# Kernel tuning notes

Hardware: AMD Instinct MI355X
Metric: run time of the kernel (lower is better)

## Reference

```python
import math
import jax, jax.numpy as jnp
import numpy as np

T, D, H, HD, ETA, R = 4096, 1024, 8, 64, 4, 7
EPS = 1e-5


def _discounted_sum(start_state, x, discounts):
    """state[t] = state[t-1]*discounts[t] + x[t], scanned over leading axis T."""
    def step(s, xd):
        xt, dt = xd
        s = s * dt + xt
        return s, s
    _, ys = jax.lax.scan(step, start_state, (x, discounts))
    return ys  # (T, *)


def _forward(inputs, terminations, tilde_k_prev, tilde_v_prev, s_prev, tick,
             W_kqv, b_kqv, W_p, b_p, W_proj, b_proj):
    cur_seq = inputs.shape[0]
    term = terminations.astype(inputs.dtype)

    kqv = (inputs @ W_kqv + b_kqv).reshape(cur_seq, H, 5 * HD)
    keys, queries, values, beta, gammas = jnp.split(kqv, 5, axis=-1)  # each (T,H,HD)
    p = (inputs @ W_p + b_p).reshape(cur_seq, H, 3 * ETA)
    p1, p2, p3 = jnp.split(p, 3, axis=-1)  # each (T,H,ETA)

    # feature-map expansion: outer product over (eta, head_dim) -> flatten to eta*HD
    keys = jnp.einsum('chd,chn->chnd', jax.nn.relu(keys), jax.nn.relu(p1)).reshape(cur_seq, H, ETA * HD)
    queries = jnp.einsum('chd,chn->chnd', jax.nn.relu(queries), jax.nn.relu(p2)).reshape(cur_seq, H, ETA * HD)
    gammas = jnp.einsum('chd,chn->chnd', jax.nn.sigmoid(gammas), jax.nn.sigmoid(p3)).reshape(cur_seq, H, ETA * HD)
    beta = jax.nn.sigmoid(beta)  # (T,H,HD)

    ticks = tick.reshape(1, 1) + jnp.arange(1, cur_seq + 1, dtype=inputs.dtype).reshape(-1, 1)  # (T,1)->(T,R)
    omegas = jnp.linspace(-math.pi, math.pi, R).astype(inputs.dtype).reshape(1, -1)
    occil = jnp.cos(ticks * omegas)  # (T,R)

    values = values * beta
    values = values[:, None, :, :] * occil[:, :, None, None]  # (T,R,H,HD)
    keys = keys * gammas
    s = keys  # (T,H,ETA*HD)
    keys = keys[:, None, :, :] * occil[:, :, None, None]  # (T,R,H,ETA*HD)

    not_term = (1.0 - term).reshape(cur_seq, 1, 1)
    discount_gamma = (1.0 - gammas) * not_term  # (T,H,ETA*HD)
    discount_beta = (1.0 - beta) * not_term     # (T,H,HD)

    final_keys = _discounted_sum(tilde_k_prev, keys, discount_gamma[:, None])    # (T,R,H,ETA*HD)
    final_values = _discounted_sum(tilde_v_prev, values, discount_beta[:, None])  # (T,R,H,HD)
    final_s = _discounted_sum(s_prev, s, discount_gamma)                          # (T,H,ETA*HD)

    kdq = jnp.einsum('crhd,chd->crh', final_keys, queries)
    kv = jnp.einsum('crhd,crh->chd', final_values, kdq)  # sum over r
    norm = jnp.einsum('chd,chd->ch', final_s, queries)
    attn_out = kv / (2 * R * norm[..., None] + EPS)
    attn_out = attn_out.reshape(cur_seq, H * HD) @ W_proj + b_proj  # dropout p=0.0 is identity

    new_tick = tick + cur_seq
    return attn_out, final_keys[-1], final_values[-1], final_s[-1], new_tick


def setup_inputs() -> dict:
    key = jax.random.key(0)
    ks = jax.random.split(key, 5)
    return {
        'inputs': jax.random.normal(ks[0], (T, D), jnp.float32),
        'terminations': jax.random.randint(ks[1], (T,), 0, 2, jnp.int32),
        'tilde_k_prev': jnp.zeros((R, H, ETA * HD), jnp.float32),
        'tilde_v_prev': jnp.zeros((R, H, HD), jnp.float32),
        's_prev': jnp.zeros((H, ETA * HD), jnp.float32),
        'tick': jnp.ones((1,), jnp.float32),
        'W_kqv': jax.random.normal(ks[2], (D, H * HD * 5), jnp.float32) * 0.02,
        'b_kqv': jnp.zeros((H * HD * 5,), jnp.float32),
        'W_p': jax.random.normal(ks[3], (D, H * ETA * 3), jnp.float32) * 0.02,
        'b_p': jnp.zeros((H * ETA * 3,), jnp.float32),
        'W_proj': jax.random.normal(ks[4], (H * HD, D), jnp.float32) * 0.02,
        'b_proj': jnp.zeros((D,), jnp.float32),
    }


def reference(inputs, terminations, tilde_k_prev, tilde_v_prev, s_prev, tick,
              W_kqv, b_kqv, W_p, b_p, W_proj, b_proj):
    return _forward(inputs, terminations, tilde_k_prev, tilde_v_prev, s_prev, tick,
                    W_kqv, b_kqv, W_p, b_p, W_proj, b_proj)
```

## Files before the change

### kernel.cpp

```cpp
#include <hip/hip_runtime.h>
#include <hip/hip_bf16.h>
#include <math.h>

#define T_SEQ 4096
#define DIM   1024
#define NH    8
#define HDIM  64
#define ETA   4
#define NR    7
#define NKQVC 2688
#define CHUNK 16
#define NCHUNK 256

typedef __attribute__((ext_vector_type(8))) short bf16x8;
typedef __attribute__((ext_vector_type(4))) short short4v;
typedef __attribute__((ext_vector_type(4))) float f32x4;

#define KQVC_OFF    0ul
#define OCC_OFF     5505024ul
#define BTPROJ_OFF  5537792ul
#define ATTNBF_OFF  5799936ul
#define BIASC_OFF   6848512ul
#define ABF_OFF     6851328ul
#define BTCAT_OFF   8948480ul
#define YSUM_OFF    6851328ul

#define O_ATTN 0ul
#define O_FK   4194304ul
#define O_FV   4208640ul
#define O_FS   4212224ul
#define O_TICK 4214272ul

__device__ __forceinline__ float sigm(float x) { return 1.f / (1.f + __expf(-x)); }

__device__ __forceinline__ short f2bf(float f) {
  union { __hip_bfloat16 b; short s; } u;
  u.b = __float2bfloat16(f);
  return u.s;
}
__device__ __forceinline__ float bf2f(short s) {
  union { __hip_bfloat16 b; short s2; } u;
  u.s2 = s;
  return __bfloat162float(u.b);
}

__device__ __forceinline__ void gload16(const void* g, void* l) {
  __builtin_amdgcn_global_load_lds(
      (const __attribute__((address_space(1))) void*)g,
      (__attribute__((address_space(3))) void*)l, 16, 0, 0);
}

__global__ __launch_bounds__(256) void cast_f32_bf16(
    const float* __restrict__ x, short* __restrict__ y) {
  size_t i = (size_t)(blockIdx.x * 256 + threadIdx.x) * 4;
  float4 v = *(const float4*)(x + i);
  short4v o;
  o.x = f2bf(v.x); o.y = f2bf(v.y); o.z = f2bf(v.z); o.w = f2bf(v.w);
  *(short4v*)(y + i) = o;
}

__global__ __launch_bounds__(256) void transpose_cast(
    const float* __restrict__ W, short* __restrict__ Bt, int K, int N) {
  __shared__ float tile[32][33];
  int n0 = blockIdx.x * 32, k0 = blockIdx.y * 32;
  int tx = threadIdx.x, ty = threadIdx.y;
  for (int i = ty; i < 32; i += 8)
    tile[i][tx] = W[(size_t)(k0 + i) * N + n0 + tx];
  __syncthreads();
  for (int i = ty; i < 32; i += 8)
    Bt[(size_t)(n0 + i) * K + k0 + tx] = f2bf(tile[tx][i]);
}

__global__ __launch_bounds__(256) void concat_bias(
    const float* __restrict__ b_kqv, const float* __restrict__ b_p,
    float* __restrict__ bc) {
  int i = blockIdx.x * 256 + threadIdx.x;
  if (i >= NKQVC) return;
  bc[i] = (i < 2560) ? b_kqv[i] : (i < 2656 ? b_p[i - 2560] : 0.f);
}

template <int OUT_BF16>
__global__ __launch_bounds__(256) void gemm_bt_mfma(
    const short* __restrict__ A, const short* __restrict__ Bt,
    const float* __restrict__ bias, void* __restrict__ Cout,
    int M, int N, int K) {
  __shared__ __align__(16) short lds[16384];

  int nwg = gridDim.x;
  int cpx = nwg >> 3;
  int bid = blockIdx.x;
  int swz = (bid & 7) * cpx + (bid >> 3);
  int nbx = N >> 7;
  int bm0 = (swz / nbx) << 7;
  int bn0 = (swz % nbx) << 7;

  const int tid = threadIdx.x;
  const int w = tid >> 6, l = tid & 63;
  const int wm = w >> 1, wn = w & 1;
  const int fr = l & 15;
  const int fq = l >> 4;

  const int ca = w * 2;
  const short* Ag0 = A + (size_t)(bm0 + ca * 16 + (l >> 2)) * K + (l & 3) * 8;
  const short* Ag1 = Ag0 + (size_t)16 * K;
  const short* Bg0 = Bt + (size_t)(bn0 + ca * 16 + (l >> 2)) * K + (l & 3) * 8;
  const short* Bg1 = Bg0 + (size_t)16 * K;

  f32x4 acc[4][4];
#pragma unroll
  for (int mi = 0; mi < 4; ++mi)
#pragma unroll
    for (int ni = 0; ni < 4; ++ni)
#pragma unroll
      for (int r = 0; r < 4; ++r) acc[mi][ni][r] = 0.f;

  const int KT = K >> 5;
  int cur = 0;
  {
    short* la = &lds[ca * 512];
    short* lb = &lds[4096 + ca * 512];
    gload16(Ag0, la);
    gload16(Ag1, la + 512);
    gload16(Bg0, lb);
    gload16(Bg1, lb + 512);
  }
  __syncthreads();

  for (int kt = 0; kt < KT; ++kt) {
    if (kt + 1 < KT) {
      int nb = (cur ^ 1) * 8192;
      int ko = (kt + 1) * 32;
      short* la = &lds[nb + ca * 512];
      short* lb = &lds[nb + 4096 + ca * 512];
      gload16(Ag0 + ko, la);
      gload16(Ag1 + ko, la + 512);
      gload16(Bg0 + ko, lb);
      gload16(Bg1 + ko, lb + 512);
    }
    const short* ArP = &lds[cur * 8192 + (wm * 64 + fr) * 32 + fq * 8];
    const short* BrP = &lds[cur * 8192 + 4096 + (wn * 64 + fr) * 32 + fq * 8];
    bf16x8 af[4], bfv[4];
#pragma unroll
    for (int mi = 0; mi < 4; ++mi) af[mi] = *(const bf16x8*)(ArP + mi * 512);
#pragma unroll
    for (int ni = 0; ni < 4; ++ni) bfv[ni] = *(const bf16x8*)(BrP + ni * 512);
#pragma unroll
    for (int mi = 0; mi < 4; ++mi)
#pragma unroll
      for (int ni = 0; ni < 4; ++ni)
        acc[mi][ni] = __builtin_amdgcn_mfma_f32_16x16x32_bf16(
            af[mi], bfv[ni], acc[mi][ni], 0, 0, 0);
    __syncthreads();
    cur ^= 1;
  }

  if (OUT_BF16) {
#pragma unroll
    for (int ni = 0; ni < 4; ++ni) {
      int col = wn * 64 + ni * 16 + fr;
      float bz = bias[bn0 + col];
#pragma unroll
      for (int mi = 0; mi < 4; ++mi) {
        int row = wm * 64 + mi * 16 + fq * 4;
#pragma unroll
        for (int r = 0; r < 4; ++r)
          lds[(row + r) * 128 + col] = f2bf(acc[mi][ni][r] + bz);
      }
    }
    __syncthreads();
    int row = tid >> 1, half = tid & 1;
    const f32x4* src = (const f32x4*)&lds[row * 128 + half * 64];
    f32x4* dst = (f32x4*)((short*)Cout + (size_t)(bm0 + row) * N + bn0 + half * 64);
#pragma unroll
    for (int i = 0; i < 8; ++i) dst[i] = src[i];
  } else {
#pragma unroll
    for (int ni = 0; ni < 4; ++ni) {
      int col = bn0 + wn * 64 + ni * 16 + fr;
      float bz = bias[col];
#pragma unroll
      for (int mi = 0; mi < 4; ++mi) {
        int row = bm0 + wm * 64 + mi * 16 + fq * 4;
#pragma unroll
        for (int r = 0; r < 4; ++r)
          ((float*)Cout)[(size_t)(row + r) * N + col] = acc[mi][ni][r] + bz;
      }
    }
  }
}

__global__ __launch_bounds__(256) void occil_kernel(const float* __restrict__ tick,
                                                    float* __restrict__ occ) {
  int t = blockIdx.x * 256 + threadIdx.x;
  if (t >= T_SEQ) return;
  float tickt = tick[0] + (float)(t + 1);
#pragma unroll
  for (int r = 0; r < NR; ++r) {
    float om = (float)(-3.14159265358979323846 + r * (3.14159265358979323846 / 3.0));
    occ[t * 8 + r] = cosf(tickt * om);
  }
  occ[t * 8 + 7] = 0.f;
}

__global__ __launch_bounds__(128) void pass_a(
    const short* __restrict__ kqv, const float* __restrict__ occ,
    const int* __restrict__ term, float* __restrict__ ysum) {
  const int c = blockIdx.x, h = blockIdx.y;
  const int tid = threadIdx.x;
  const int w = tid >> 6, dd = tid & 63;
  const int R0 = w ? 4 : 0;
  const int RN = w ? 3 : 4;
  __shared__ float sp[CHUNK][12];
  __shared__ float socc[CHUNK][8];
  __shared__ float snt[CHUNK];
  for (int i = tid; i < CHUNK * 12; i += 128) {
    int t = i / 12, j = i - t * 12;
    sp[t][j] = bf2f(kqv[(size_t)(c * CHUNK + t) * NKQVC + 2560 + h * 12 + j]);
  }
  for (int i = tid; i < CHUNK * 8; i += 128)
    socc[i >> 3][i & 7] = occ[(size_t)c * CHUNK * 8 + i];
  for (int t = tid; t < CHUNK; t += 128)
    snt[t] = 1.f - (float)term[c * CHUNK + t];
  __syncthreads();

  float yk[4][ETA], yv[4], ys[ETA], Pg[ETA], Pb = 1.f;
#pragma unroll
  for (int rr = 0; rr < 4; ++rr) {
    yv[rr] = 0.f;
#pragma unroll
    for (int n = 0; n < ETA; ++n) yk[rr][n] = 0.f;
  }
#pragma unroll
  for (int n = 0; n < ETA; ++n) { ys[n] = 0.f; Pg[n] = 1.f; }

  size_t bcur = (size_t)(c * CHUNK) * NKQVC + h * 320 + dd;
  short ck = kqv[bcur], cv = kqv[bcur + 128], cbt = kqv[bcur + 192], cg = kqv[bcur + 256];
  for (int t = 0; t < CHUNK; ++t) {
    size_t bnx = bcur + (t < CHUNK - 1 ? NKQVC : 0);
    short nk = kqv[bnx], nv = kqv[bnx + 128], nbt = kqv[bnx + 192], ng = kqv[bnx + 256];

    float nt = snt[t];
    float rk = fmaxf(bf2f(ck), 0.f);
    float sg = sigm(bf2f(cg));
    float sb = sigm(bf2f(cbt));
    float occr[4];
#pragma unroll
    for (int rr = 0; rr < 4; ++rr) occr[rr] = socc[t][R0 + rr];
#pragma unroll
    for (int n = 0; n < ETA; ++n) {
      float rp1 = fmaxf(sp[t][n], 0.f);
      float sp3 = sigm(sp[t][8 + n]);
      float gam = sg * sp3;
      float xs  = rk * rp1 * gam;
      float dg  = (1.f - gam) * nt;
      if (w) {
        Pg[n] *= dg;
        ys[n] = fmaf(ys[n], dg, xs);
      }
#pragma unroll
      for (int rr = 0; rr < 4; ++rr)
        if (rr < RN) yk[rr][n] = fmaf(yk[rr][n], dg, xs * occr[rr]);
    }
    float vb = bf2f(cv) * sb;
    float db = (1.f - sb) * nt;
    if (!w) Pb *= db;
#pragma unroll
    for (int rr = 0; rr < 4; ++rr)
      if (rr < RN) yv[rr] = fmaf(yv[rr], db, vb * occr[rr]);

    ck = nk; cv = nv; cbt = nbt; cg = ng; bcur = bnx;
  }

  float* o = ysum + (size_t)(c * NH + h) * 44 * 64 + dd;
#pragma unroll
  for (int rr = 0; rr < 4; ++rr)
    if (rr < RN) {
#pragma unroll
      for (int n = 0; n < ETA; ++n) o[((R0 + rr) * 4 + n) * 64] = yk[rr][n];
      o[(28 + R0 + rr) * 64] = yv[rr];
    }
  if (w) {
#pragma unroll
    for (int n = 0; n < ETA; ++n) o[(35 + n) * 64] = ys[n];
#pragma unroll
    for (int n = 0; n < ETA; ++n) o[(39 + n) * 64] = Pg[n];
  } else {
    o[43 * 64] = Pb;
  }
}

__global__ __launch_bounds__(256) void pass_b(
    float* __restrict__ ysum, const float* __restrict__ k_prev,
    const float* __restrict__ v_prev, const float* __restrict__ s_prev) {
  int idx = blockIdx.x * 256 + threadIdx.x;
  int dd = idx & 63;
  int slot = (idx >> 6) % 39;
  int h = idx / (39 * 64);

  int pslot;
  float f;
  if (slot < 28) {
    int r = slot >> 2, n = slot & 3;
    f = k_prev[(size_t)(r * NH + h) * 256 + n * 64 + dd];
    pslot = 39 + n;
  } else if (slot < 35) {
    int r = slot - 28;
    f = v_prev[(size_t)(r * NH + h) * 64 + dd];
    pslot = 43;
  } else {
    int n = slot - 35;
    f = s_prev[(size_t)h * 256 + n * 64 + dd];
    pslot = 39 + n;
  }
  const size_t STRIDE = (size_t)NH * 2816;
  float* yb = ysum + (size_t)h * 2816 + slot * 64 + dd;
  const float* pb = ysum + (size_t)h * 2816 + pslot * 64 + dd;

#define PD 16
  float yring[PD], pring[PD];
#pragma unroll
  for (int d = 0; d < PD; ++d) {
    yring[d] = yb[(size_t)d * STRIDE];
    pring[d] = pb[(size_t)d * STRIDE];
  }
  const int NB = NCHUNK / PD;
  for (int cb = 0; cb < NB; ++cb) {
    int c0 = cb * PD;
    float ynext[PD], pnext[PD];
    if (cb + 1 < NB) {
#pragma unroll
      for (int j = 0; j < PD; ++j) {
        ynext[j] = yb[(size_t)(c0 + PD + j) * STRIDE];
        pnext[j] = pb[(size_t)(c0 + PD + j) * STRIDE];
      }
    }
#pragma unroll
    for (int j = 0; j < PD; ++j) {
      yb[(size_t)(c0 + j) * STRIDE] = f;
      f = fmaf(f, pring[j], yring[j]);
    }
    if (cb + 1 < NB) {
#pragma unroll
      for (int j = 0; j < PD; ++j) { yring[j] = ynext[j]; pring[j] = pnext[j]; }
    }
  }
#undef PD
}

__global__ __launch_bounds__(128) void pass_c(
    const short* __restrict__ kqv, const float* __restrict__ occ,
    const int* __restrict__ term, const float* __restrict__ carry,
    short* __restrict__ attn, float* __restrict__ out,
    const float* __restrict__ tick) {
  const int c = blockIdx.x, h = blockIdx.y;
  const int tid = threadIdx.x;
  const int w = tid >> 6, dd = tid & 63;
  const int R0 = w ? 4 : 0;
  const int RN = w ? 3 : 4;
  __shared__ float sp[CHUNK][12];
  __shared__ float socc[CHUNK][8];
  __shared__ float snt[CHUNK];
  __shared__ float xch[2][2][64];
  for (int i = tid; i < CHUNK * 12; i += 128) {
    int t = i / 12, j = i - t * 12;
    sp[t][j] = bf2f(kqv[(size_t)(c * CHUNK + t) * NKQVC + 2560 + h * 12 + j]);
  }
  for (int i = tid; i < CHUNK * 8; i += 128)
    socc[i >> 3][i & 7] = occ[(size_t)c * CHUNK * 8 + i];
  for (int t = tid; t < CHUNK; t += 128)
    snt[t] = 1.f - (float)term[c * CHUNK + t];

  const float* cp = carry + (size_t)(c * NH + h) * 2816 + dd;
  float fk[4][ETA], fv[4], fs[ETA];
#pragma unroll
  for (int rr = 0; rr < 4; ++rr)
    if (rr < RN) {
#pragma unroll
      for (int n = 0; n < ETA; ++n) fk[rr][n] = cp[((R0 + rr) * 4 + n) * 64];
      fv[rr] = cp[(28 + R0 + rr) * 64];
    }
  if (w) {
#pragma unroll
    for (int n = 0; n < ETA; ++n) fs[n] = cp[(35 + n) * 64];
  }
  __syncthreads();

  size_t bcur = (size_t)(c * CHUNK) * NKQVC + h * 320 + dd;
  short ck = kqv[bcur], cq = kqv[bcur + 64], cv = kqv[bcur + 128],
        cbt = kqv[bcur + 192], cg = kqv[bcur + 256];
  for (int t = 0; t < CHUNK; ++t) {
    size_t bnx = bcur + (t < CHUNK - 1 ? NKQVC : 0);
    short nk = kqv[bnx], nq = kqv[bnx + 64], nv = kqv[bnx + 128],
          nbt = kqv[bnx + 192], ng = kqv[bnx + 256];

    float nt = snt[t];
    float rk = fmaxf(bf2f(ck), 0.f);
    float rq = fmaxf(bf2f(cq), 0.f);
    float sg = sigm(bf2f(cg));
    float sb = sigm(bf2f(cbt));
    float occr[4];
#pragma unroll
    for (int rr = 0; rr < 4; ++rr) occr[rr] = socc[t][R0 + rr];
    float kdqp[4] = {0.f, 0.f, 0.f, 0.f};
    float normp = 0.f;
#pragma unroll
    for (int n = 0; n < ETA; ++n) {
      float rp1 = fmaxf(sp[t][n], 0.f);
      float rp2 = fmaxf(sp[t][4 + n], 0.f);
      float sp3 = sigm(sp[t][8 + n]);
      float gam = sg * sp3;
      float xs  = rk * rp1 * gam;
      float dg  = (1.f - gam) * nt;
      float qf  = rq * rp2;
      if (w) {
        fs[n] = fmaf(fs[n], dg, xs);
        normp = fmaf(fs[n], qf, normp);
      }
#pragma unroll
      for (int rr = 0; rr < 4; ++rr)
        if (rr < RN) {
          fk[rr][n] = fmaf(fk[rr][n], dg, xs * occr[rr]);
          kdqp[rr]  = fmaf(fk[rr][n], qf, kdqp[rr]);
        }
    }
    float vb = bf2f(cv) * sb;
    float db = (1.f - sb) * nt;
#pragma unroll
    for (int rr = 0; rr < 4; ++rr)
      if (rr < RN) fv[rr] = fmaf(fv[rr], db, vb * occr[rr]);

    float red[4];
    red[0] = kdqp[0]; red[1] = kdqp[1]; red[2] = kdqp[2];
    red[3] = w ? normp : kdqp[3];
#pragma unroll
    for (int i = 0; i < 4; ++i) {
      float x = red[i];
#pragma unroll
      for (int m = 1; m < 64; m <<= 1) x += __shfl_xor(x, m, 64);
      red[i] = x;
    }
    int par = t & 1;
    if (w) {
      float kvv1 = fv[0] * red[0];
      kvv1 = fmaf(fv[1], red[1], kvv1);
      kvv1 = fmaf(fv[2], red[2], kvv1);
      float denom = fmaf(14.f, red[3], 1e-5f);
      xch[par][0][dd] = kvv1;
      xch[par][1][dd] = denom;
    }
    __syncthreads();
    if (!w) {
      float kvv = fv[0] * red[0];
      kvv = fmaf(fv[1], red[1], kvv);
      kvv = fmaf(fv[2], red[2], kvv);
      kvv = fmaf(fv[3], red[3], kvv);
      kvv += xch[par][0][dd];
      attn[(size_t)(c * CHUNK + t) * 512 + h * 64 + dd] = f2bf(kvv / xch[par][1][dd]);
    }

    ck = nk; cq = nq; cv = nv; cbt = nbt; cg = ng; bcur = bnx;
  }

  if (c == NCHUNK - 1) {
#pragma unroll
    for (int rr = 0; rr < 4; ++rr)
      if (rr < RN) {
#pragma unroll
        for (int n = 0; n < ETA; ++n)
          out[O_FK + (size_t)((R0 + rr) * NH + h) * 256 + n * 64 + dd] = fk[rr][n];
        out[O_FV + (size_t)((R0 + rr) * NH + h) * 64 + dd] = fv[rr];
      }
    if (w) {
#pragma unroll
      for (int n = 0; n < ETA; ++n)
        out[O_FS + (size_t)h * 256 + n * 64 + dd] = fs[n];
    }
    if (!w && h == 0 && dd == 0) out[O_TICK] = tick[0] + (float)T_SEQ;
  }
}

extern "C" void kernel_launch(void* const* d_in, const int* in_sizes, int n_in,
                              void* d_out, int out_size, void* d_ws, size_t ws_size,
                              hipStream_t stream) {
  const float* inputs = (const float*)d_in[0];
  const int*   term   = (const int*)d_in[1];
  const float* k_prev = (const float*)d_in[2];
  const float* v_prev = (const float*)d_in[3];
  const float* s_prev = (const float*)d_in[4];
  const float* tick   = (const float*)d_in[5];
  const float* W_kqv  = (const float*)d_in[6];
  const float* b_kqv  = (const float*)d_in[7];
  const float* W_p    = (const float*)d_in[8];
  const float* b_p    = (const float*)d_in[9];
  const float* W_proj = (const float*)d_in[10];
  const float* b_proj = (const float*)d_in[11];
  float* out = (float*)d_out;
  float* ws  = (float*)d_ws;

  short* kqvc   = (short*)(ws + KQVC_OFF);
  float* occ    = ws + OCC_OFF;
  short* BtProj = (short*)(ws + BTPROJ_OFF);
  short* attnbf = (short*)(ws + ATTNBF_OFF);
  float* biasc  = ws + BIASC_OFF;
  short* Abf    = (short*)(ws + ABF_OFF);
  short* BtCat  = (short*)(ws + BTCAT_OFF);
  float* ysum   = ws + YSUM_OFF;

  cast_f32_bf16<<<4096, 256, 0, stream>>>(inputs, Abf);
  transpose_cast<<<dim3(80, 32), dim3(32, 8), 0, stream>>>(W_kqv, BtCat, 1024, 2560);
  transpose_cast<<<dim3(3, 32), dim3(32, 8), 0, stream>>>(
      W_p, BtCat + (size_t)2560 * 1024, 1024, 96);
  transpose_cast<<<dim3(32, 16), dim3(32, 8), 0, stream>>>(W_proj, BtProj, 512, 1024);
  concat_bias<<<11, 256, 0, stream>>>(b_kqv, b_p, biasc);

  occil_kernel<<<16, 256, 0, stream>>>(tick, occ);

  gemm_bt_mfma<1><<<672, 256, 0, stream>>>(Abf, BtCat, biasc, kqvc,
                                           T_SEQ, NKQVC, DIM);

  pass_a<<<dim3(NCHUNK, NH), 128, 0, stream>>>(kqvc, occ, term, ysum);
  pass_b<<<78, 256, 0, stream>>>(ysum, k_prev, v_prev, s_prev);
  pass_c<<<dim3(NCHUNK, NH), 128, 0, stream>>>(kqvc, occ, term, ysum,
                                               attnbf, out, tick);

  gemm_bt_mfma<0><<<256, 256, 0, stream>>>(attnbf, BtProj, b_proj, out,
                                           T_SEQ, DIM, NH * HDIM);
}
```

Before: 151.3 us.

## Split scan passes across four waves and defer cross-wave reduction to chunk end

Pass_a and pass_c now run with 256 threads per block, so each wave handles two (or one) of the seven R rotations instead of four or three, with wave 3 also carrying the s-state and decay products. In pass_c the per-timestep __syncthreads exchange is replaced by writing per-wave partial numerators and the denominator into a shared buffer indexed by timestep, then reducing once after the chunk loop. This aims to shorten the serial dependence chain per thread and remove sixteen barriers per block. In exchange every wave redundantly recomputes the shared gate and sigmoid terms and reloads the kqv stream, and shared memory use grows to about 20KB per block.

Result: slower. 177.5 us (+17.3%).

```diff
diff --git a/kernel.cpp b/kernel.cpp
--- a/kernel.cpp
+++ b/kernel.cpp
@@ -202,30 +202,31 @@
   occ[t * 8 + 7] = 0.f;
 }
 
-__global__ __launch_bounds__(128) void pass_a(
+__global__ __launch_bounds__(256) void pass_a(
     const short* __restrict__ kqv, const float* __restrict__ occ,
     const int* __restrict__ term, float* __restrict__ ysum) {
   const int c = blockIdx.x, h = blockIdx.y;
   const int tid = threadIdx.x;
   const int w = tid >> 6, dd = tid & 63;
-  const int R0 = w ? 4 : 0;
-  const int RN = w ? 3 : 4;
+  const int R0 = w * 2;
+  const int RN = (w == 3) ? 1 : 2;
+  const bool w3 = (w == 3);
   __shared__ float sp[CHUNK][12];
   __shared__ float socc[CHUNK][8];
   __shared__ float snt[CHUNK];
-  for (int i = tid; i < CHUNK * 12; i += 128) {
+  for (int i = tid; i < CHUNK * 12; i += 256) {
     int t = i / 12, j = i - t * 12;
     sp[t][j] = bf2f(kqv[(size_t)(c * CHUNK + t) * NKQVC + 2560 + h * 12 + j]);
   }
-  for (int i = tid; i < CHUNK * 8; i += 128)
+  for (int i = tid; i < CHUNK * 8; i += 256)
     socc[i >> 3][i & 7] = occ[(size_t)c * CHUNK * 8 + i];
-  for (int t = tid; t < CHUNK; t += 128)
+  for (int t = tid; t < CHUNK; t += 256)
     snt[t] = 1.f - (float)term[c * CHUNK + t];
   __syncthreads();
 
-  float yk[4][ETA], yv[4], ys[ETA], Pg[ETA], Pb = 1.f;
-#pragma unroll
-  for (int rr = 0; rr < 4; ++rr) {
+  float yk[2][ETA], yv[2], ys[ETA], Pg[ETA], Pb = 1.f;
+#pragma unroll
+  for (int rr = 0; rr < 2; ++rr) {
     yv[rr] = 0.f;
 #pragma unroll
     for (int n = 0; n < ETA; ++n) yk[rr][n] = 0.f;
@@ -243,9 +244,10 @@
     float rk = fmaxf(bf2f(ck), 0.f);
     float sg = sigm(bf2f(cg));
     float sb = sigm(bf2f(cbt));
-    float occr[4];
-#pragma unroll
-    for (int rr = 0; rr < 4; ++rr) occr[rr] = socc[t][R0 + rr];
+    float occr[2];
+#pragma unroll
+    for (int rr = 0; rr < 2; ++rr)
+      occr[rr] = socc[t][(R0 + rr) < 7 ? (R0 + rr) : 7];
 #pragma unroll
     for (int n = 0; n < ETA; ++n) {
       float rp1 = fmaxf(sp[t][n], 0.f);
@@ -253,19 +255,19 @@
       float gam = sg * sp3;
       float xs  = rk * rp1 * gam;
       float dg  = (1.f - gam) * nt;
-      if (w) {
+      if (w3) {
         Pg[n] *= dg;
         ys[n] = fmaf(ys[n], dg, xs);
       }
 #pragma unroll
-      for (int rr = 0; rr < 4; ++rr)
+      for (int rr = 0; rr < 2; ++rr)
         if (rr < RN) yk[rr][n] = fmaf(yk[rr][n], dg, xs * occr[rr]);
     }
     float vb = bf2f(cv) * sb;
     float db = (1.f - sb) * nt;
-    if (!w) Pb *= db;
-#pragma unroll
-    for (int rr = 0; rr < 4; ++rr)
+    if (w3) Pb *= db;
+#pragma unroll
+    for (int rr = 0; rr < 2; ++rr)
       if (rr < RN) yv[rr] = fmaf(yv[rr], db, vb * occr[rr]);
 
     ck = nk; cv = nv; cbt = nbt; cg = ng; bcur = bnx;
@@ -273,18 +275,17 @@
 
   float* o = ysum + (size_t)(c * NH + h) * 44 * 64 + dd;
 #pragma unroll
-  for (int rr = 0; rr < 4; ++rr)
+  for (int rr = 0; rr < 2; ++rr)
     if (rr < RN) {
 #pragma unroll
       for (int n = 0; n < ETA; ++n) o[((R0 + rr) * 4 + n) * 64] = yk[rr][n];
       o[(28 + R0 + rr) * 64] = yv[rr];
     }
-  if (w) {
+  if (w3) {
 #pragma unroll
     for (int n = 0; n < ETA; ++n) o[(35 + n) * 64] = ys[n];
 #pragma unroll
     for (int n = 0; n < ETA; ++n) o[(39 + n) * 64] = Pg[n];
-  } else {
     o[43 * 64] = Pb;
   }
 }
@@ -347,7 +348,7 @@
 #undef PD
 }
 
-__global__ __launch_bounds__(128) void pass_c(
+__global__ __launch_bounds__(256) void pass_c(
     const short* __restrict__ kqv, const float* __restrict__ occ,
     const int* __restrict__ term, const float* __restrict__ carry,
     short* __restrict__ attn, float* __restrict__ out,
@@ -355,31 +356,32 @@
   const int c = blockIdx.x, h = blockIdx.y;
   const int tid = threadIdx.x;
   const int w = tid >> 6, dd = tid & 63;
-  const int R0 = w ? 4 : 0;
-  const int RN = w ? 3 : 4;
+  const int R0 = w * 2;
+  const int RN = (w == 3) ? 1 : 2;
+  const bool w3 = (w == 3);
   __shared__ float sp[CHUNK][12];
   __shared__ float socc[CHUNK][8];
   __shared__ float snt[CHUNK];
-  __shared__ float xch[2][2][64];
-  for (int i = tid; i < CHUNK * 12; i += 128) {
+  __shared__ float xch[5][CHUNK][64];
+  for (int i = tid; i < CHUNK * 12; i += 256) {
     int t = i / 12, j = i - t * 12;
     sp[t][j] = bf2f(kqv[(size_t)(c * CHUNK + t) * NKQVC + 2560 + h * 12 + j]);
   }
-  for (int i = tid; i < CHUNK * 8; i += 128)
+  for (int i = tid; i < CHUNK * 8; i += 256)
     socc[i >> 3][i & 7] = occ[(size_t)c * CHUNK * 8 + i];
-  for (int t = tid; t < CHUNK; t += 128)
+  for (int t = tid; t < CHUNK; t += 256)
     snt[t] = 1.f - (float)term[c * CHUNK + t];
 
   const float* cp = carry + (size_t)(c * NH + h) * 2816 + dd;
-  float fk[4][ETA], fv[4], fs[ETA];
-#pragma unroll
-  for (int rr = 0; rr < 4; ++rr)
+  float fk[2][ETA], fv[2], fs[ETA];
+#pragma unroll
+  for (int rr = 0; rr < 2; ++rr)
     if (rr < RN) {
 #pragma unroll
       for (int n = 0; n < ETA; ++n) fk[rr][n] = cp[((R0 + rr) * 4 + n) * 64];
       fv[rr] = cp[(28 + R0 + rr) * 64];
     }
-  if (w) {
+  if (w3) {
 #pragma unroll
     for (int n = 0; n < ETA; ++n) fs[n] = cp[(35 + n) * 64];
   }
@@ -398,10 +400,11 @@
     float rq = fmaxf(bf2f(cq), 0.f);
     float sg = sigm(bf2f(cg));
     float sb = sigm(bf2f(cbt));
-    float occr[4];
-#pragma unroll
-    for (int rr = 0; rr < 4; ++rr) occr[rr] = socc[t][R0 + rr];
-    float kdqp[4] = {0.f, 0.f, 0.f, 0.f};
+    float occr[2];
+#pragma unroll
+    for (int rr = 0; rr < 2; ++rr)
+      occr[rr] = socc[t][(R0 + rr) < 7 ? (R0 + rr) : 7];
+    float kdqp[2] = {0.f, 0.f};
     float normp = 0.f;
 #pragma unroll
     for (int n = 0; n < ETA; ++n) {
@@ -412,12 +415,12 @@
       float xs  = rk * rp1 * gam;
       float dg  = (1.f - gam) * nt;
       float qf  = rq * rp2;
-      if (w) {
+      if (w3) {
         fs[n] = fmaf(fs[n], dg, xs);
         normp = fmaf(fs[n], qf, normp);
       }
 #pragma unroll
-      for (int rr = 0; rr < 4; ++rr)
+      for (int rr = 0; rr < 2; ++rr)
         if (rr < RN) {
           fk[rr][n] = fmaf(fk[rr][n], dg, xs * occr[rr]);
           kdqp[rr]  = fmaf(fk[rr][n], qf, kdqp[rr]);
@@ -426,56 +429,50 @@
     float vb = bf2f(cv) * sb;
     float db = (1.f - sb) * nt;
 #pragma unroll
-    for (int rr = 0; rr < 4; ++rr)
+    for (int rr = 0; rr < 2; ++rr)
       if (rr < RN) fv[rr] = fmaf(fv[rr], db, vb * occr[rr]);
 
-    float red[4];
-    red[0] = kdqp[0]; red[1] = kdqp[1]; red[2] = kdqp[2];
-    red[3] = w ? normp : kdqp[3];
-#pragma unroll
-    for (int i = 0; i < 4; ++i) {
+    float red[2];
+    red[0] = kdqp[0];
+    red[1] = w3 ? normp : kdqp[1];
+#pragma unroll
+    for (int i = 0; i < 2; ++i) {
       float x = red[i];
 #pragma unroll
       for (int m = 1; m < 64; m <<= 1) x += __shfl_xor(x, m, 64);
       red[i] = x;
     }
-    int par = t & 1;
-    if (w) {
-      float kvv1 = fv[0] * red[0];
-      kvv1 = fmaf(fv[1], red[1], kvv1);
-      kvv1 = fmaf(fv[2], red[2], kvv1);
-      float denom = fmaf(14.f, red[3], 1e-5f);
-      xch[par][0][dd] = kvv1;
-      xch[par][1][dd] = denom;
-    }
-    __syncthreads();
-    if (!w) {
-      float kvv = fv[0] * red[0];
-      kvv = fmaf(fv[1], red[1], kvv);
-      kvv = fmaf(fv[2], red[2], kvv);
-      kvv = fmaf(fv[3], red[3], kvv);
-      kvv += xch[par][0][dd];
-      attn[(size_t)(c * CHUNK + t) * 512 + h * 64 + dd] = f2bf(kvv / xch[par][1][dd]);
-    }
+    float kvvP = fv[0] * red[0];
+    if (!w3) kvvP = fmaf(fv[1], red[1], kvvP);
+    xch[w][t][dd] = kvvP;
+    if (w3) xch[4][t][dd] = fmaf(14.f, red[1], 1e-5f);
 
     ck = nk; cq = nq; cv = nv; cbt = nbt; cg = ng; bcur = bnx;
   }
+  __syncthreads();
+
+#pragma unroll
+  for (int j = 0; j < 4; ++j) {
+    int t = w * 4 + j;
+    float kvv = xch[0][t][dd] + xch[1][t][dd] + xch[2][t][dd] + xch[3][t][dd];
+    attn[(size_t)(c * CHUNK + t) * 512 + h * 64 + dd] = f2bf(kvv / xch[4][t][dd]);
+  }
 
   if (c == NCHUNK - 1) {
 #pragma unroll
-    for (int rr = 0; rr < 4; ++rr)
+    for (int rr = 0; rr < 2; ++rr)
       if (rr < RN) {
 #pragma unroll
         for (int n = 0; n < ETA; ++n)
           out[O_FK + (size_t)((R0 + rr) * NH + h) * 256 + n * 64 + dd] = fk[rr][n];
         out[O_FV + (size_t)((R0 + rr) * NH + h) * 64 + dd] = fv[rr];
       }
-    if (w) {
+    if (w3) {
 #pragma unroll
       for (int n = 0; n < ETA; ++n)
         out[O_FS + (size_t)h * 256 + n * 64 + dd] = fs[n];
     }
-    if (!w && h == 0 && dd == 0) out[O_TICK] = tick[0] + (float)T_SEQ;
+    if (w == 0 && h == 0 && dd == 0) out[O_TICK] = tick[0] + (float)T_SEQ;
   }
 }
 
@@ -518,9 +515,9 @@
   gemm_bt_mfma<1><<<672, 256, 0, stream>>>(Abf, BtCat, biasc, kqvc,
                                            T_SEQ, NKQVC, DIM);
 
-  pass_a<<<dim3(NCHUNK, NH), 128, 0, stream>>>(kqvc, occ, term, ysum);
+  pass_a<<<dim3(NCHUNK, NH), 256, 0, stream>>>(kqvc, occ, term, ysum);
   pass_b<<<78, 256, 0, stream>>>(ysum, k_prev, v_prev, s_prev);
-  pass_c<<<dim3(NCHUNK, NH), 128, 0, stream>>>(kqvc, occ, term, ysum,
+  pass_c<<<dim3(NCHUNK, NH), 256, 0, stream>>>(kqvc, occ, term, ysum,
                                                attnbf, out, tick);
 
   gemm_bt_mfma<0><<<256, 256, 0, stream>>>(attnbf, BtProj, b_proj, out,
```
